# Kernel tuning notes

Hardware: AMD Instinct MI355X
Metric: run time of the kernel (lower is better)

The kernel has to match this reference:

```python
import jax, jax.numpy as jnp
import numpy as np

B, C, H, W = 16, 2048, 16, 16
HEADS = 4
HEAD_DIM = C // HEADS


def setup_inputs() -> dict:
    key = jax.random.key(0)
    ks = jax.random.split(key, 7)
    s = 0.02
    x = jax.random.normal(ks[0], (B, C, H, W), dtype=jnp.float32)
    q_w = jax.random.normal(ks[1], (HEADS, HEAD_DIM, C), dtype=jnp.float32) * s
    q_b = jax.random.normal(ks[2], (HEADS, HEAD_DIM), dtype=jnp.float32) * s
    k_w = jax.random.normal(ks[3], (HEADS, HEAD_DIM, C), dtype=jnp.float32) * s
    k_b = jax.random.normal(ks[4], (HEADS, HEAD_DIM), dtype=jnp.float32) * s
    v_w = jax.random.normal(ks[5], (HEADS, C, C), dtype=jnp.float32) * s
    v_b = jax.random.normal(ks[6], (HEADS, C), dtype=jnp.float32) * s
    return {"x": x, "q_w": q_w, "q_b": q_b, "k_w": k_w, "k_b": k_b, "v_w": v_w, "v_b": v_b}


def reference(x, q_w, q_b, k_w, k_b, v_w, v_b):
    b, c, h, w = x.shape
    heads, head_dim, _ = q_w.shape
    # [B, N, C] with N = H*W
    patch = jnp.transpose(x, (0, 2, 3, 1)).reshape(b, h * w, c)
    # stacked per-head linear projections (bias per head)
    Q = jnp.einsum('bnc,hdc->bhnd', patch, q_w) + q_b[None, :, None, :]   # [B,heads,N,head_dim]
    K = jnp.einsum('bnc,hdc->bhnd', patch, k_w) + k_b[None, :, None, :]   # [B,heads,N,head_dim]
    V = jnp.einsum('bnc,hec->bhne', patch, v_w) + v_b[None, :, None, :]   # [B,heads,N,C]
    sim = jnp.einsum('bhqd,bhkd->bhqk', Q, K) / (head_dim ** 0.5)          # [B,heads,N,N]
    # sum over query dim, softmax over heads
    att = jnp.sum(sim, axis=2)[:, :, None, :]                              # [B,heads,1,N]
    att = jax.nn.softmax(att, axis=1)
    n = att.shape[-1]
    side = int(n ** 0.5)
    attention_score = att.reshape(b, heads, side, side)                    # [B,heads,h,w]
    # per-head spatial gating of the input, concatenated along channels
    x_enhance = (attention_score[:, :, None, :, :] * x[:, None, :, :, :]).reshape(b, heads * c, h, w)
    # standard softmax attention combine
    sim = jax.nn.softmax(sim, axis=-1)
    general = jnp.einsum('bhqk,bhke->bhqe', sim, V)                        # [B,heads,N,C]
    general = general.reshape(b, heads, side, side, c)
    general = jnp.transpose(general, (0, 1, 4, 2, 3)).reshape(b, heads * c, side, side)
    output = general + x_enhance
    return (attention_score, output)
```

## Files before the change

kernel.cpp:

```cpp
#include <hip/hip_runtime.h>
#include <hip/hip_bf16.h>

#define B_ 16
#define C_ 2048
#define N_ 256
#define HEADS_ 4
#define D_ 512

typedef unsigned int u32;
typedef unsigned short ushort_t;
typedef __attribute__((ext_vector_type(8))) short bfx8;
typedef __attribute__((ext_vector_type(4))) float fx4;

__device__ __forceinline__ unsigned short f2bs(float f) {
    __hip_bfloat16 h = __float2bfloat16(f);
    return __builtin_bit_cast(unsigned short, h);
}
__device__ __forceinline__ float bs2f(ushort_t u) {
    u32 v = ((u32)u) << 16;
    return __builtin_bit_cast(float, v);
}
__device__ __forceinline__ void gload16(const void* g, void* l) {
    __builtin_amdgcn_global_load_lds((const __attribute__((address_space(1))) u32*)g,
                                     (__attribute__((address_space(3))) u32*)l, 16, 0, 0);
}
__device__ __forceinline__ int xcd_swz(int bid, int nwg) {
    return (bid & 7) * (nwg >> 3) + (bid >> 3);
}

#define VMW8() asm volatile("s_waitcnt vmcnt(8)" ::: "memory")
#define SBAR() __builtin_amdgcn_s_barrier()
#define SCB0() __builtin_amdgcn_sched_barrier(0)

#define STAGE8(MAT, BUF, KH, J) do {                                          \
    const ushort_t* s_ = (MAT) ? Bm : A;                                      \
    _Pragma("unroll")                                                         \
    for (int l_ = 0; l_ < 2; ++l_) {                                          \
        const int r_ = l_ * 128 + (tid >> 2);                                 \
        const int k_ = (J) * 64 + (KH) * 32 + (((tid & 3) ^ ((tid >> 3) & 3)) * 8); \
        gload16(s_ + (size_t)r_ * K + k_,                                     \
                (char*)(&lds[MAT][BUF][KH][0][0]) + l_ * 8192 + tid * 16);    \
    } } while (0)

#define LDA8(dst, BUF, KH, MH) do {                                           \
    _Pragma("unroll")                                                         \
    for (int i_ = 0; i_ < 4; ++i_)                                            \
        dst[i_] = *(const bfx8*)&lds[0][BUF][KH][wmr + (MH) * 64 + i_ * 16 + l16][swz8]; \
    } while (0)

#define LDB8(dst, BUF, KH) do {                                               \
    _Pragma("unroll")                                                         \
    for (int i_ = 0; i_ < 4; ++i_)                                            \
        dst[i_] = *(const bfx8*)&lds[1][BUF][KH][wnr + i_ * 16 + l16][swz8];  \
    } while (0)

#define MM8(aa, bb, MH) do {                                                  \
    __builtin_amdgcn_s_setprio(1);                                            \
    _Pragma("unroll")                                                         \
    for (int i_ = 0; i_ < 4; ++i_) {                                          \
        _Pragma("unroll")                                                     \
        for (int n_ = 0; n_ < 4; ++n_)                                        \
            acc[(MH) * 4 + i_][n_] = __builtin_amdgcn_mfma_f32_16x16x32_bf16( \
                aa[i_], bb[n_], acc[(MH) * 4 + i_][n_], 0, 0, 0);             \
    }                                                                         \
    __builtin_amdgcn_s_setprio(0);                                            \
} while (0)

typedef ushort_t lds256_t[2][2][2][256][32];

__device__ __forceinline__ void gemm256_8ph(const ushort_t* __restrict__ A,
                                            const ushort_t* __restrict__ Bm,
                                            int K, lds256_t& lds, fx4 acc[8][4])
{
    const int tid = threadIdx.x;
    const int lane = tid & 63;
    const int w = tid >> 6;
    const int l16 = lane & 15, lhi = lane >> 4;
    const int swz8 = (lhi ^ ((l16 >> 1) & 3)) * 8;
    const int wmr = (w >> 2) * 128;
    const int wnr = (w & 3) * 64;
    const int nkt = K >> 6;

    STAGE8(0, 0, 0, 0); STAGE8(1, 0, 0, 0);
    STAGE8(0, 0, 1, 0); STAGE8(1, 0, 1, 0);
    STAGE8(0, 1, 0, 1); STAGE8(1, 1, 0, 1);
    VMW8();
    SBAR();

    for (int j = 0; j < nkt; ++j) {
        const int b = j & 1;
        const int js1 = (j + 1 < nkt) ? j + 1 : j;
        const int js2 = (j + 2 < nkt) ? j + 2 : j;
        bfx8 a0[4], a1[4], b0[4], b1[4];
        LDA8(a0, b, 0, 0);
        LDB8(b0, b, 0);
        STAGE8(0, b ^ 1, 1, js1);
        SBAR();
        MM8(a0, b0, 0);
        SCB0();
        SBAR();
        LDA8(a1, b, 0, 1);
        STAGE8(1, b ^ 1, 1, js1);
        SBAR();
        MM8(a1, b0, 1);
        SCB0();
        VMW8();
        SBAR();
        LDA8(a0, b, 1, 0);
        LDB8(b1, b, 1);
        STAGE8(0, b, 0, js2);
        SBAR();
        MM8(a0, b1, 0);
        SCB0();
        SBAR();
        LDA8(a1, b, 1, 1);
        STAGE8(1, b, 0, js2);
        SBAR();
        MM8(a1, b1, 1);
        SCB0();
        VMW8();
        SBAR();
    }
}

#define EPI256_IDX() \
    const int lane = threadIdx.x & 63, w = threadIdx.x >> 6; \
    const int l16 = lane & 15, lhi = lane >> 4; \
    const int wmr = (w >> 2) * 128, wnr = (w & 3) * 64;

__device__ __forceinline__ void mfma_core(const ushort_t* __restrict__ A,
                                          const ushort_t* __restrict__ Bm,
                                          int K, fx4 acc[4][4])
{
    __shared__ __align__(16) ushort_t As[128 * 32];
    __shared__ __align__(16) ushort_t Bs[128 * 32];
    const int tid = threadIdx.x;
    const int lane = tid & 63, wave = tid >> 6;
    const int l16 = lane & 15, lhi = lane >> 4;
    const int swz8 = (lhi ^ ((l16 >> 1) & 3)) * 8;
    const int wm = (wave >> 1) * 64, wn = (wave & 1) * 64;

    for (int k0 = 0; k0 < K; k0 += 32) {
        const int f0 = tid, f1 = tid + 256;
        gload16(A + (size_t)(f0 >> 2) * K + k0 + (((f0 & 3) ^ ((f0 >> 3) & 3)) * 8), As + f0 * 8);
        gload16(A + (size_t)(f1 >> 2) * K + k0 + (((f1 & 3) ^ ((f1 >> 3) & 3)) * 8), As + f1 * 8);
        gload16(Bm + (size_t)(f0 >> 2) * K + k0 + (((f0 & 3) ^ ((f0 >> 3) & 3)) * 8), Bs + f0 * 8);
        gload16(Bm + (size_t)(f1 >> 2) * K + k0 + (((f1 & 3) ^ ((f1 >> 3) & 3)) * 8), Bs + f1 * 8);
        __syncthreads();
        bfx8 af[4], bfr[4];
#pragma unroll
        for (int i = 0; i < 4; ++i)
            af[i] = *(const bfx8*)(As + (wm + i * 16 + l16) * 32 + swz8);
#pragma unroll
        for (int j = 0; j < 4; ++j)
            bfr[j] = *(const bfx8*)(Bs + (wn + j * 16 + l16) * 32 + swz8);
#pragma unroll
        for (int i = 0; i < 4; ++i)
#pragma unroll
            for (int j = 0; j < 4; ++j)
                acc[i][j] = __builtin_amdgcn_mfma_f32_16x16x32_bf16(af[i], bfr[j], acc[i][j], 0, 0, 0);
        __syncthreads();
    }
}

#define EPI_IDX() \
    const int lane = threadIdx.x & 63, wave = threadIdx.x >> 6; \
    const int l16 = lane & 15, lhi = lane >> 4; \
    const int wm = (wave >> 1) * 64, wn = (wave & 1) * 64;

__global__ __launch_bounds__(256) void k_castw(const float* __restrict__ s, ushort_t* __restrict__ d, int n) {
    int i = (blockIdx.x * 256 + threadIdx.x) * 4;
    if (i >= n) return;
    float4 v = *(const float4*)(s + i);
    ushort4 o = { f2bs(v.x), f2bs(v.y), f2bs(v.z), f2bs(v.w) };
    *(ushort4*)(d + i) = o;
}

__global__ __launch_bounds__(256) void k_cast_x(const float* __restrict__ x,
                                                ushort_t* __restrict__ xb, ushort_t* __restrict__ xbT,
                                                float* __restrict__ xpart) {
    __shared__ float t[32][33];
    const int b = blockIdx.z, c0 = blockIdx.y * 32, n0 = blockIdx.x * 32;
    const int tn = threadIdx.x & 31, tc8 = threadIdx.x >> 5;
    const float* xp = x + ((size_t)b * C_ + c0) * N_ + n0;
#pragma unroll
    for (int p = 0; p < 4; ++p) {
        int cc = tc8 + p * 8;
        float v = xp[(size_t)cc * N_ + tn];
        t[cc][tn] = v;
        xb[((size_t)b * C_ + c0 + cc) * N_ + n0 + tn] = f2bs(v);
        float s = v;
#pragma unroll
        for (int o = 16; o; o >>= 1) s += __shfl_xor(s, o, 32);
        if (tn == 0) xpart[(size_t)blockIdx.x * B_ * C_ + (size_t)b * C_ + c0 + cc] = s;
    }
    __syncthreads();
#pragma unroll
    for (int p = 0; p < 4; ++p) {
        int nn = tc8 + p * 8;
        xbT[((size_t)b * N_ + n0 + nn) * C_ + c0 + tn] = f2bs(t[tn][nn]);
    }
}

__global__ __launch_bounds__(256) void k_xsum2(const float* __restrict__ xpart, float* __restrict__ xsum) {
    const int c = blockIdx.x * 256 + threadIdx.x, b = blockIdx.y;
    float s = 0.f;
#pragma unroll
    for (int t = 0; t < 8; ++t) s += xpart[(size_t)t * B_ * C_ + (size_t)b * C_ + c];
    xsum[(size_t)b * C_ + c] = s;
}

__global__ __launch_bounds__(256) void k_qsum(const float* __restrict__ xsum, const float* __restrict__ qw,
                                              const float* __restrict__ qb, float* __restrict__ qsum) {
    const int wave = threadIdx.x >> 6, lane = threadIdx.x & 63;
    const int row = blockIdx.x * 4 + wave;
    const int h = row >> 9, d = row & 511;
    const float* wr = qw + (size_t)row * C_;
    float acc[16];
#pragma unroll
    for (int bb = 0; bb < 16; ++bb) acc[bb] = 0.f;
    for (int it = 0; it < C_ / 64; ++it) {
        const int c = it * 64 + lane;
        const float w = wr[c];
#pragma unroll
        for (int bb = 0; bb < 16; ++bb) acc[bb] += xsum[(size_t)bb * C_ + c] * w;
    }
#pragma unroll
    for (int bb = 0; bb < 16; ++bb) {
        float s = acc[bb];
#pragma unroll
        for (int o = 32; o; o >>= 1) s += __shfl_xor(s, o, 64);
        if (lane == 0) qsum[(size_t)((bb << 2) | h) * D_ + d] = s + 256.0f * qb[row];
    }
}

__global__ __launch_bounds__(64) void k_const(const float* __restrict__ qsum, const float* __restrict__ kb,
                                              float* __restrict__ cst) {
    const int bh = blockIdx.x, h = bh & 3, lane = threadIdx.x;
    float s = 0.f;
    for (int d = lane; d < D_; d += 64) s += qsum[(size_t)bh * D_ + d] * kb[h * D_ + d];
#pragma unroll
    for (int o = 32; o; o >>= 1) s += __shfl_xor(s, o, 64);
    if (lane == 0) cst[bh] = s;
}

__global__ __launch_bounds__(256) void k_vecp(const float* __restrict__ qsum, const float* __restrict__ kw,
                                              float* __restrict__ partv) {
    const int ct = blockIdx.x, h = blockIdx.y, dsl = blockIdx.z;
    __shared__ float qs[16 * 128];
    for (int i = threadIdx.x; i < 16 * 128; i += 256) {
        int bb = i >> 7, dd = i & 127;
        qs[i] = qsum[(size_t)((bb << 2) | h) * D_ + dsl * 128 + dd];
    }
    __syncthreads();
    const int c = ct * 256 + threadIdx.x;
    const float* wp = kw + ((size_t)h * D_ + dsl * 128) * C_ + c;
    float acc[16];
#pragma unroll
    for (int bb = 0; bb < 16; ++bb) acc[bb] = 0.f;
    for (int dd = 0; dd < 128; ++dd) {
        const float w = wp[(size_t)dd * C_];
#pragma unroll
        for (int bb = 0; bb < 16; ++bb) acc[bb] += qs[bb * 128 + dd] * w;
    }
#pragma unroll
    for (int bb = 0; bb < 16; ++bb)
        partv[((size_t)dsl * 64 + ((bb << 2) | h)) * C_ + c] = acc[bb];
}

__global__ __launch_bounds__(256) void k_att(const float* __restrict__ x, const float* __restrict__ partv,
                                             float* __restrict__ part) {
    const int bh = blockIdx.x, sl = blockIdx.y, b = bh >> 2;
    __shared__ float vs[512];
    const int c0 = sl * 512;
    for (int i = threadIdx.x; i < 512; i += 256) {
        float v = 0.f;
#pragma unroll
        for (int dsl = 0; dsl < 4; ++dsl) v += partv[((size_t)dsl * 64 + bh) * C_ + c0 + i];
        vs[i] = v;
    }
    __syncthreads();
    float a = 0.f;
    const float* xp = x + ((size_t)b * C_ + c0) * N_ + threadIdx.x;
#pragma unroll 8
    for (int c = 0; c < 512; ++c) a += vs[c] * xp[(size_t)c * N_];
    part[((size_t)sl * 64 + bh) * N_ + threadIdx.x] = a;
}

__global__ __launch_bounds__(256) void k_score(const float* __restrict__ part, const float* __restrict__ cst,
                                               float* __restrict__ score, float* __restrict__ out0) {
    const int b = blockIdx.x, k = threadIdx.x;
    const float scale = 0.044194173824159216f;
    float a[4];
#pragma unroll
    for (int h = 0; h < 4; ++h) {
        const int bh = b * 4 + h;
        float s = cst[bh];
#pragma unroll
        for (int sl = 0; sl < 4; ++sl) s += part[((size_t)sl * 64 + bh) * N_ + k];
        a[h] = s * scale;
    }
    float mx = fmaxf(fmaxf(a[0], a[1]), fmaxf(a[2], a[3]));
    float e0 = expf(a[0] - mx), e1 = expf(a[1] - mx), e2 = expf(a[2] - mx), e3 = expf(a[3] - mx);
    float inv = 1.0f / (e0 + e1 + e2 + e3);
    float r[4] = { e0 * inv, e1 * inv, e2 * inv, e3 * inv };
#pragma unroll
    for (int h = 0; h < 4; ++h) {
        score[(size_t)(b * 4 + h) * N_ + k] = r[h];
        out0[(size_t)(b * 4 + h) * N_ + k] = r[h];
    }
}

__global__ __launch_bounds__(512, 2) void k_proj(const ushort_t* __restrict__ xbT,
                                                 const ushort_t* __restrict__ qwb, const ushort_t* __restrict__ kwb,
                                                 const float* __restrict__ qb, const float* __restrict__ kb,
                                                 ushort_t* __restrict__ QKbuf) {
    __shared__ __align__(16) lds256_t lds;
    const int wg = xcd_swz(blockIdx.x, 256);
    const int quad = wg >> 2;
    const int mt = quad >> 2;
    const int nt = (quad & 3) * 4 + (wg & 3);
    const int c0 = nt * 256;
    const int qk = c0 >> 11;
    const int rem = c0 & 2047;
    const ushort_t* A  = xbT + (size_t)mt * 256 * C_;
    const ushort_t* Bm = (qk ? kwb : qwb) + (size_t)rem * C_;
    const float* bias  = (qk ? kb : qb) + rem;
    const int K = C_;

    fx4 acc[8][4];
#pragma unroll
    for (int i = 0; i < 8; ++i)
#pragma unroll
        for (int j = 0; j < 4; ++j) acc[i][j] = (fx4){0.f, 0.f, 0.f, 0.f};
    gemm256_8ph(A, Bm, K, lds, acc);

    EPI256_IDX();
#pragma unroll
    for (int i = 0; i < 8; ++i)
#pragma unroll
        for (int n = 0; n < 4; ++n)
#pragma unroll
            for (int r = 0; r < 4; ++r) {
                const int gr = mt * 256 + wmr + i * 16 + lhi * 4 + r;
                const int bq = gr >> 8, nn = gr & 255;
                const int lc = wnr + n * 16 + l16;
                const int hh = (rem + lc) >> 9, dl = (rem + lc) & 511;
                const float v = acc[i][n][r] + bias[lc];
                QKbuf[((((size_t)(qk * 16 + bq) * 4 + hh) * 256) + nn) * 512 + dl] = f2bs(v);
            }
}

__global__ __launch_bounds__(512, 2) void k_out(const ushort_t* __restrict__ vwb, const float* __restrict__ vb,
                                                const ushort_t* __restrict__ Tt, const float* __restrict__ score,
                                                const ushort_t* __restrict__ xb, float* __restrict__ out1) {
    __shared__ __align__(16) lds256_t lds;
    const int wg = xcd_swz(blockIdx.x, 512);
    const int h = wg >> 7, l = wg & 127;
    const int quad = l >> 2;
    const int mt = quad >> 2;
    const int nt = (quad & 3) * 4 + (l & 3);
    const ushort_t* A  = vwb + (size_t)h * C_ * C_ + (size_t)mt * 256 * C_;
    const ushort_t* Bm = Tt + (size_t)h * 16 * N_ * C_ + (size_t)nt * 256 * C_;
    const int K = C_;

    fx4 acc[8][4];
#pragma unroll
    for (int i = 0; i < 8; ++i)
#pragma unroll
        for (int j = 0; j < 4; ++j) acc[i][j] = (fx4){0.f, 0.f, 0.f, 0.f};
    gemm256_8ph(A, Bm, K, lds, acc);

    EPI256_IDX();
#pragma unroll
    for (int i = 0; i < 8; ++i)
#pragma unroll
        for (int n = 0; n < 4; ++n)
#pragma unroll
            for (int r = 0; r < 4; ++r) {
                const int e = mt * 256 + wmr + i * 16 + lhi * 4 + r;
                const int col = nt * 256 + wnr + n * 16 + l16;
                const int b = col >> 8, nn = col & 255;
                float v = acc[i][n][r] + vb[h * C_ + e]
                        + score[(size_t)(b * 4 + h) * N_ + nn] * bs2f(xb[((size_t)b * C_ + e) * N_ + nn]);
                out1[((size_t)(b * 4 + h) * C_ + e) * N_ + nn] = v;
            }
}

__global__ __launch_bounds__(256) void k_sim(const ushort_t* __restrict__ QKbuf, float* __restrict__ simf) {
    const int wg = blockIdx.x;
    const int bh = wg >> 2, mt = (wg >> 1) & 1, ntl = wg & 1;
    const ushort_t* Qr = QKbuf;
    const ushort_t* Kr = QKbuf + (size_t)16 * 4 * 256 * 512;
    const ushort_t* A = Qr + ((size_t)bh * 256 + mt * 128) * 512;
    const ushort_t* Bm = Kr + ((size_t)bh * 256 + ntl * 128) * 512;

    fx4 acc[4][4];
#pragma unroll
    for (int i = 0; i < 4; ++i)
#pragma unroll
        for (int j = 0; j < 4; ++j) acc[i][j] = (fx4){0.f, 0.f, 0.f, 0.f};
    mfma_core(A, Bm, D_, acc);

    EPI_IDX();
    const float scale = 0.044194173824159216f;
#pragma unroll
    for (int i = 0; i < 4; ++i)
#pragma unroll
        for (int j = 0; j < 4; ++j)
#pragma unroll
            for (int r = 0; r < 4; ++r) {
                const int q = mt * 128 + wm + i * 16 + lhi * 4 + r;
                const int k = ntl * 128 + wn + j * 16 + l16;
                simf[(size_t)bh * N_ * N_ + (size_t)q * N_ + k] = acc[i][j][r] * scale;
            }
}

__global__ __launch_bounds__(64) void k_softP(const float* __restrict__ simf, ushort_t* __restrict__ Pb) {
    const size_t row = blockIdx.x;
    const float* p = simf + row * N_;
    ushort_t* o = Pb + row * N_;
    const int t = threadIdx.x;
    float v0 = p[t], v1 = p[t + 64], v2 = p[t + 128], v3 = p[t + 192];
    float mx = fmaxf(fmaxf(v0, v1), fmaxf(v2, v3));
#pragma unroll
    for (int off = 32; off; off >>= 1) mx = fmaxf(mx, __shfl_xor(mx, off, 64));
    float e0 = expf(v0 - mx), e1 = expf(v1 - mx), e2 = expf(v2 - mx), e3 = expf(v3 - mx);
    float s = e0 + e1 + e2 + e3;
#pragma unroll
    for (int off = 32; off; off >>= 1) s += __shfl_xor(s, off, 64);
    const float inv = 1.0f / s;
    o[t] = f2bs(e0 * inv); o[t + 64] = f2bs(e1 * inv);
    o[t + 128] = f2bs(e2 * inv); o[t + 192] = f2bs(e3 * inv);
}

__global__ __launch_bounds__(256) void k_T(const ushort_t* __restrict__ Pb, const ushort_t* __restrict__ xb,
                                           ushort_t* __restrict__ Tt) {
    const int wg = xcd_swz(blockIdx.x, 2048);
    const int b = wg >> 7, l = wg & 127;
    const int mt = l >> 4, nt = l & 15;
    const ushort_t* A = Pb + ((size_t)b * 1024 + mt * 128) * 256;
    const ushort_t* Bm = xb + ((size_t)b * 2048 + nt * 128) * 256;

    fx4 acc[4][4];
#pragma unroll
    for (int i = 0; i < 4; ++i)
#pragma unroll
        for (int j = 0; j < 4; ++j) acc[i][j] = (fx4){0.f, 0.f, 0.f, 0.f};
    mfma_core(A, Bm, N_, acc);

    EPI_IDX();
#pragma unroll
    for (int i = 0; i < 4; ++i)
#pragma unroll
        for (int j = 0; j < 4; ++j)
#pragma unroll
            for (int r = 0; r < 4; ++r) {
                const int rowm = mt * 128 + wm + i * 16 + lhi * 4 + r;
                const int h = rowm >> 8, q = rowm & 255;
                const int c = nt * 128 + wn + j * 16 + l16;
                Tt[(((size_t)h * 16 + b) * 256 + q) * 2048 + c] = f2bs(acc[i][j][r]);
            }
}

extern "C" void kernel_launch(void* const* d_in, const int* in_sizes, int n_in,
                              void* d_out, int out_size, void* d_ws, size_t ws_size,
                              hipStream_t stream)
{
    const float* x  = (const float*)d_in[0];
    const float* qw = (const float*)d_in[1];
    const float* qb = (const float*)d_in[2];
    const float* kw = (const float*)d_in[3];
    const float* kb = (const float*)d_in[4];
    const float* vw = (const float*)d_in[5];
    const float* vb = (const float*)d_in[6];

    float* out0 = (float*)d_out;
    float* out1 = out0 + (size_t)B_ * HEADS_ * N_;

    char* w = (char*)d_ws;
    ushort_t* vwb  = (ushort_t*)w;  w += (size_t)4 * C_ * C_ * 2;
    ushort_t* qwb  = (ushort_t*)w;  w += (size_t)4 * D_ * C_ * 2;
    ushort_t* kwb  = (ushort_t*)w;  w += (size_t)4 * D_ * C_ * 2;
    ushort_t* xb   = (ushort_t*)w;  w += (size_t)B_ * C_ * N_ * 2;
    ushort_t* QKbuf= (ushort_t*)w;  w += (size_t)2 * 16 * 4 * 256 * 512 * 2;
    ushort_t* Pb   = (ushort_t*)w;  w += (size_t)64 * N_ * N_ * 2;
    float*    simf = (float*)w;     w += (size_t)64 * N_ * N_ * 4;
    ushort_t* Tt   = (ushort_t*)w;  w += (size_t)64 * N_ * C_ * 2;
    ushort_t* xbT  = Tt;
    float*    xpart= (float*)w;     w += (size_t)8 * B_ * C_ * 4;
    float*    xsum = (float*)w;     w += (size_t)B_ * C_ * 4;
    float*    qsum = (float*)w;     w += (size_t)64 * D_ * 4;
    float*    cst  = (float*)w;     w += 1024;
    float*    partv= (float*)w;     w += (size_t)4 * 64 * C_ * 4;
    float*    part = (float*)w;     w += (size_t)4 * 64 * N_ * 4;
    float*    score= (float*)w;     w += (size_t)64 * N_ * 4;

    k_castw<<<dim3(4 * D_ * C_ / 4 / 256), 256, 0, stream>>>(qw, qwb, 4 * D_ * C_);
    k_castw<<<dim3(4 * D_ * C_ / 4 / 256), 256, 0, stream>>>(kw, kwb, 4 * D_ * C_);
    k_castw<<<dim3(4 * C_ * C_ / 4 / 256), 256, 0, stream>>>(vw, vwb, 4 * C_ * C_);
    k_cast_x<<<dim3(8, 64, 16), 256, 0, stream>>>(x, xb, xbT, xpart);

    k_xsum2<<<dim3(8, 16), 256, 0, stream>>>(xpart, xsum);
    k_qsum <<<dim3(512), 256, 0, stream>>>(xsum, qw, qb, qsum);
    k_const<<<dim3(64), 64, 0, stream>>>(qsum, kb, cst);
    k_vecp <<<dim3(8, 4, 4), 256, 0, stream>>>(qsum, kw, partv);
    k_att  <<<dim3(64, 4), 256, 0, stream>>>(x, partv, part);
    k_score<<<dim3(16), 256, 0, stream>>>(part, cst, score, out0);

    k_proj <<<dim3(256), 512, 0, stream>>>(xbT, qwb, kwb, qb, kb, QKbuf);
    k_sim  <<<dim3(256), 256, 0, stream>>>(QKbuf, simf);
    k_softP<<<dim3(64 * N_), 64, 0, stream>>>(simf, Pb);
    k_T    <<<dim3(2048), 256, 0, stream>>>(Pb, xb, Tt);
    k_out  <<<dim3(512), 512, 0, stream>>>(vwb, vb, Tt, score, xb, out1);
}
```

Before: 387.8 us.

## Use 256x256 8-wave GEMM for P·x and unroll pipelined k-loop by two

```diff
diff --git a/kernel.cpp b/kernel.cpp
--- a/kernel.cpp
+++ b/kernel.cpp
@@ -30,7 +30,8 @@
 
 #define VMW8() asm volatile("s_waitcnt vmcnt(8)" ::: "memory")
 #define SBAR() __builtin_amdgcn_s_barrier()
-#define SCB0() __builtin_amdgcn_sched_barrier(0)
+#define LGKM0() do { asm volatile("s_waitcnt lgkmcnt(0)" ::: "memory"); \
+                     __builtin_amdgcn_sched_barrier(0); } while (0)
 
 #define STAGE8(MAT, BUF, KH, J) do {                                          \
     const ushort_t* s_ = (MAT) ? Bm : A;                                      \
@@ -64,6 +65,36 @@
                 aa[i_], bb[n_], acc[(MH) * 4 + i_][n_], 0, 0, 0);             \
     }                                                                         \
     __builtin_amdgcn_s_setprio(0);                                            \
+} while (0)
+
+#define KTILE(BUF, JS1, JS2) do {                                             \
+    bfx8 a0[4], a1[4], b0[4], b1[4];                                          \
+                                                       \
+    LDA8(a0, BUF, 0, 0); LDB8(b0, BUF, 0);                                    \
+    STAGE8(0, BUF ^ 1, 1, JS1);                                               \
+    SBAR(); LGKM0();                                                          \
+    MM8(a0, b0, 0);                                                           \
+    SBAR();                                                                   \
+                                                       \
+    LDA8(a1, BUF, 0, 1);                                                      \
+    STAGE8(1, BUF ^ 1, 1, JS1);                                               \
+    SBAR(); LGKM0();                                                          \
+    MM8(a1, b0, 1);                                                           \
+    VMW8();                                                                   \
+    SBAR();                                                                   \
+                                                       \
+    LDA8(a0, BUF, 1, 0); LDB8(b1, BUF, 1);                                    \
+    STAGE8(0, BUF, 0, JS2);                                                   \
+    SBAR(); LGKM0();                                                          \
+    MM8(a0, b1, 0);                                                           \
+    SBAR();                                                                   \
+                                                       \
+    LDA8(a1, BUF, 1, 1);                                                      \
+    STAGE8(1, BUF, 0, JS2);                                                   \
+    SBAR(); LGKM0();                                                          \
+    MM8(a1, b1, 1);                                                           \
+    VMW8();                                                                   \
+    SBAR();                                                                   \
 } while (0)
 
 typedef ushort_t lds256_t[2][2][2][256][32];
@@ -87,39 +118,13 @@
     VMW8();
     SBAR();
 
-    for (int j = 0; j < nkt; ++j) {
-        const int b = j & 1;
-        const int js1 = (j + 1 < nkt) ? j + 1 : j;
-        const int js2 = (j + 2 < nkt) ? j + 2 : j;
-        bfx8 a0[4], a1[4], b0[4], b1[4];
-        LDA8(a0, b, 0, 0);
-        LDB8(b0, b, 0);
-        STAGE8(0, b ^ 1, 1, js1);
-        SBAR();
-        MM8(a0, b0, 0);
-        SCB0();
-        SBAR();
-        LDA8(a1, b, 0, 1);
-        STAGE8(1, b ^ 1, 1, js1);
-        SBAR();
-        MM8(a1, b0, 1);
-        SCB0();
-        VMW8();
-        SBAR();
-        LDA8(a0, b, 1, 0);
-        LDB8(b1, b, 1);
-        STAGE8(0, b, 0, js2);
-        SBAR();
-        MM8(a0, b1, 0);
-        SCB0();
-        SBAR();
-        LDA8(a1, b, 1, 1);
-        STAGE8(1, b, 0, js2);
-        SBAR();
-        MM8(a1, b1, 1);
-        SCB0();
-        VMW8();
-        SBAR();
+    for (int jj = 0; jj < nkt; jj += 2) {
+        const int js1a = jj + 1;
+        const int js2a = (jj + 2 < nkt) ? jj + 2 : nkt - 1;
+        const int js1b = js2a;
+        const int js2b = (jj + 3 < nkt) ? jj + 3 : nkt - 1;
+        KTILE(0, js1a, js2a);
+        KTILE(1, js1b, js2b);
     }
 }
 
@@ -387,6 +392,37 @@
             }
 }
 
+__global__ __launch_bounds__(512, 2) void k_T8(const ushort_t* __restrict__ Pb, const ushort_t* __restrict__ xb,
+                                               ushort_t* __restrict__ Tt) {
+    __shared__ __align__(16) lds256_t lds;
+    const int wg = xcd_swz(blockIdx.x, 512);
+    const int b = wg >> 5, l = wg & 31;
+    const int mt = l >> 3, nt = l & 7;
+    const ushort_t* A  = Pb + ((size_t)b * 1024 + mt * 256) * 256;
+    const ushort_t* Bm = xb + ((size_t)b * 2048 + nt * 256) * 256;
+    const int K = N_;
+
+    fx4 acc[8][4];
+#pragma unroll
+    for (int i = 0; i < 8; ++i)
+#pragma unroll
+        for (int j = 0; j < 4; ++j) acc[i][j] = (fx4){0.f, 0.f, 0.f, 0.f};
+    gemm256_8ph(A, Bm, K, lds, acc);
+
+    EPI256_IDX();
+#pragma unroll
+    for (int i = 0; i < 8; ++i)
+#pragma unroll
+        for (int n = 0; n < 4; ++n)
+#pragma unroll
+            for (int r = 0; r < 4; ++r) {
+                const int rowm = mt * 256 + wmr + i * 16 + lhi * 4 + r;
+                const int h = rowm >> 8, q = rowm & 255;
+                const int c = nt * 256 + wnr + n * 16 + l16;
+                Tt[(((size_t)h * 16 + b) * 256 + q) * 2048 + c] = f2bs(acc[i][n][r]);
+            }
+}
+
 __global__ __launch_bounds__(256) void k_sim(const ushort_t* __restrict__ QKbuf, float* __restrict__ simf) {
     const int wg = blockIdx.x;
     const int bh = wg >> 2, mt = (wg >> 1) & 1, ntl = wg & 1;
@@ -432,35 +468,6 @@
     const float inv = 1.0f / s;
     o[t] = f2bs(e0 * inv); o[t + 64] = f2bs(e1 * inv);
     o[t + 128] = f2bs(e2 * inv); o[t + 192] = f2bs(e3 * inv);
-}
-
-__global__ __launch_bounds__(256) void k_T(const ushort_t* __restrict__ Pb, const ushort_t* __restrict__ xb,
-                                           ushort_t* __restrict__ Tt) {
-    const int wg = xcd_swz(blockIdx.x, 2048);
-    const int b = wg >> 7, l = wg & 127;
-    const int mt = l >> 4, nt = l & 15;
-    const ushort_t* A = Pb + ((size_t)b * 1024 + mt * 128) * 256;
-    const ushort_t* Bm = xb + ((size_t)b * 2048 + nt * 128) * 256;
-
-    fx4 acc[4][4];
-#pragma unroll
-    for (int i = 0; i < 4; ++i)
-#pragma unroll
-        for (int j = 0; j < 4; ++j) acc[i][j] = (fx4){0.f, 0.f, 0.f, 0.f};
-    mfma_core(A, Bm, N_, acc);
-
-    EPI_IDX();
-#pragma unroll
-    for (int i = 0; i < 4; ++i)
-#pragma unroll
-        for (int j = 0; j < 4; ++j)
-#pragma unroll
-            for (int r = 0; r < 4; ++r) {
-                const int rowm = mt * 128 + wm + i * 16 + lhi * 4 + r;
-                const int h = rowm >> 8, q = rowm & 255;
-                const int c = nt * 128 + wn + j * 16 + l16;
-                Tt[(((size_t)h * 16 + b) * 256 + q) * 2048 + c] = f2bs(acc[i][j][r]);
-            }
 }
 
 extern "C" void kernel_launch(void* const* d_in, const int* in_sizes, int n_in,
@@ -511,6 +518,6 @@
     k_proj <<<dim3(256), 512, 0, stream>>>(xbT, qwb, kwb, qb, kb, QKbuf);
     k_sim  <<<dim3(256), 256, 0, stream>>>(QKbuf, simf);
     k_softP<<<dim3(64 * N_), 64, 0, stream>>>(simf, Pb);
-    k_T    <<<dim3(2048), 256, 0, stream>>>(Pb, xb, Tt);
+    k_T8   <<<dim3(512), 512, 0, stream>>>(Pb, xb, Tt);
     k_out  <<<dim3(512), 512, 0, stream>>>(vwb, vb, Tt, score, xb, out1);
 }
```

Measured after the change: 386.6 us. Within noise of the previous version (-0.3%).
